# Optimization experiments

Measured on AMD Instinct MI355X. Metric: run time of the kernel, lower is better.

Reference implementation:

```python
import jax, jax.numpy as jnp
import numpy as np

TEMP = 0.5  # matches init_kwargs temperature


def setup_inputs() -> dict:
    key = jax.random.key(0)
    k1, k2 = jax.random.split(key)
    B, D = 4096, 256
    return {
        "z_i": jax.random.normal(k1, (B, D), dtype=jnp.float32),
        "z_j": jax.random.normal(k2, (B, D), dtype=jnp.float32),
    }


def reference(z_i, z_j):
    B = z_i.shape[0]
    N = 2 * B
    z = jnp.concatenate([z_i, z_j], axis=0)          # [N, D]
    sim = (z @ z.T) / TEMP                            # [N, N]

    # Faithful to source: BOTH positive halves come from diag(sim, +B)
    pos = jnp.concatenate([jnp.diagonal(sim, offset=B)] * 2)  # [N]

    # Arithmetic mask: exclude diagonal and the +/-B off-diagonals (static)
    idx = np.arange(N)
    mask = (idx[:, None] != idx[None, :]) & (np.abs(idx[:, None] - idx[None, :]) != B)
    neg = jnp.where(jnp.asarray(mask), sim, -jnp.inf)          # [N, N]

    # logits = [pos | negatives], label = 0 -> CE_i = lse(logits_i) - pos_i
    logits = jnp.concatenate([pos[:, None], neg], axis=1)      # [N, N+1]
    lse = jax.nn.logsumexp(logits, axis=1)                     # [N]
    loss = jnp.mean(lse - pos) / N                             # CE mean, then /N as in source
    return loss
```

## Files before the change

kernel.cpp:

```cpp
#include <hip/hip_runtime.h>
#include <hip/hip_bf16.h>

#define DD 256
#define NN 8192
#define B_ROWS 4096
#define G 64
#define NPAIRS 2080
#define M_FIX 160.0f
#define SCALE 1.6986436f
#define LN2 0.69314718055994531f

typedef __attribute__((ext_vector_type(8))) short bf16x8;
typedef __attribute__((ext_vector_type(4))) float f32x4;

__device__ __forceinline__ unsigned short f2bf(float f) {
    unsigned int x = __float_as_uint(f);
    x += 0x7fffu + ((x >> 16) & 1u);
    return (unsigned short)(x >> 16);
}
__device__ __forceinline__ float bf2f(unsigned short u) {
    return __uint_as_float((unsigned int)u << 16);
}
__device__ __forceinline__ float exp2_raw(float x) {
    float r; asm("v_exp_f32 %0, %1" : "=v"(r) : "v"(x)); return r;
}
__device__ __forceinline__ void gload16(const unsigned short* g, unsigned short* l) {
    __builtin_amdgcn_global_load_lds(
        (const __attribute__((address_space(1))) void*)g,
        (__attribute__((address_space(3))) void*)l, 16, 0, 0);
}

__global__ void cast_pos_kernel(const float* __restrict__ zi, const float* __restrict__ zj,
                                unsigned short* __restrict__ zb, float* __restrict__ pos) {
    const int w = threadIdx.x >> 6;
    const int l = threadIdx.x & 63;
    const int r = blockIdx.x * 4 + w;
    const float4 a = ((const float4*)(zi + (size_t)r * DD))[l];
    const float4 b = ((const float4*)(zj + (size_t)r * DD))[l];
    float d = a.x * b.x + a.y * b.y + a.z * b.z + a.w * b.w;
    #pragma unroll
    for (int off = 32; off > 0; off >>= 1) d += __shfl_down(d, off, 64);
    if (l == 0) pos[r] = 2.0f * d;
    ushort4 oa, ob;
    oa.x = f2bf(a.x * SCALE); oa.y = f2bf(a.y * SCALE);
    oa.z = f2bf(a.z * SCALE); oa.w = f2bf(a.w * SCALE);
    ob.x = f2bf(b.x * SCALE); ob.y = f2bf(b.y * SCALE);
    ob.z = f2bf(b.z * SCALE); ob.w = f2bf(b.w * SCALE);
    ((ushort4*)(zb + (size_t)r * DD))[l] = oa;
    ((ushort4*)(zb + (size_t)(r + B_ROWS) * DD))[l] = ob;
}

__global__ __launch_bounds__(128, 2) void simlse_kernel(const unsigned short* __restrict__ zb,
                                                        unsigned short* __restrict__ P) {
    __shared__ unsigned short tile[64 * DD];
    const int tid = threadIdx.x;
    const int w  = tid >> 6;
    const int l  = tid & 63;
    const int lg = l >> 4;
    const int lr = l & 15;

    int b = blockIdx.x, g1 = 0;
    while (b >= G - g1) { b -= G - g1; ++g1; }
    const int g2 = g1 + b;
    const int rbase = g1 * 128 + w * 64;
    const int cbase = g2 * 128;
    const bool diag = (g1 == g2);

    bf16x8 aF[4][8];
    #pragma unroll
    for (int rt = 0; rt < 4; ++rt) {
        const unsigned short* ap = zb + (size_t)(rbase + rt * 16 + lr) * DD + lg * 8;
        #pragma unroll
        for (int ks = 0; ks < 8; ++ks) aF[rt][ks] = *(const bf16x8*)(ap + ks * 32);
    }

    float rs[4][4];
    #pragma unroll
    for (int rt = 0; rt < 4; ++rt)
        #pragma unroll
        for (int j = 0; j < 4; ++j) rs[rt][j] = 0.f;
    float cs[8];
    #pragma unroll
    for (int k = 0; k < 8; ++k) cs[k] = 0.f;

    #pragma unroll
    for (int t = 0; t < 2; ++t) {
        const int c0 = cbase + t * 64;
        __syncthreads();
        #pragma unroll
        for (int j = 0; j < 16; ++j) {
            const int slot = w * 16 + j;
            const int s = slot >> 3, ks = slot & 7;
            gload16(zb + (size_t)(c0 + s * 16 + lr) * DD + ks * 32 + lg * 8,
                    tile + slot * 512);
        }
        __syncthreads();
        #pragma unroll
        for (int s = 0; s < 4; ++s) {
            f32x4 acc[4];
            #pragma unroll
            for (int rt = 0; rt < 4; ++rt) acc[rt] = (f32x4){0.f, 0.f, 0.f, 0.f};
            #pragma unroll
            for (int ks = 0; ks < 8; ++ks) {
                bf16x8 bF = *(const bf16x8*)(tile + (s * 8 + ks) * 512 + l * 8);
                #pragma unroll
                for (int rt = 0; rt < 4; ++rt)
                    acc[rt] = __builtin_amdgcn_mfma_f32_16x16x32_bf16(aF[rt][ks], bF, acc[rt], 0, 0, 0);
            }
            float csum = 0.f;
            #pragma unroll
            for (int rt = 0; rt < 4; ++rt) {
                const bool dtile = diag && (w * 4 + rt == t * 4 + s);
                #pragma unroll
                for (int j = 0; j < 4; ++j) {
                    float e = exp2_raw(acc[rt][j] - M_FIX);
                    if (dtile && (lr == lg * 4 + j)) e = 0.f;
                    rs[rt][j] += e;
                    csum += e;
                }
            }
            cs[t * 4 + s] = csum;
        }
    }

    #pragma unroll
    for (int rt = 0; rt < 4; ++rt)
        #pragma unroll
        for (int j = 0; j < 4; ++j) {
            float v = rs[rt][j];
            v += __shfl_xor(v, 1, 64);
            v += __shfl_xor(v, 2, 64);
            v += __shfl_xor(v, 4, 64);
            v += __shfl_xor(v, 8, 64);
            rs[rt][j] = v;
        }
    if (lr == 0) {
        #pragma unroll
        for (int rt = 0; rt < 4; ++rt)
            #pragma unroll
            for (int j = 0; j < 4; ++j) {
                const int row = rbase + rt * 16 + lg * 4 + j;
                P[(size_t)row * G + g2] = f2bf(rs[rt][j]);
            }
    }

    if (!diag) {
        #pragma unroll
        for (int k = 0; k < 8; ++k) {
            float v = cs[k];
            v += __shfl_xor(v, 16, 64);
            v += __shfl_xor(v, 32, 64);
            cs[k] = v;
        }
        __syncthreads();
        float* red = (float*)tile;
        if (lg == 0) {
            #pragma unroll
            for (int k = 0; k < 8; ++k) red[(w * 8 + k) * 16 + lr] = cs[k];
        }
        __syncthreads();
        const int k2 = tid >> 4, lr2 = tid & 15;
        float v = red[k2 * 16 + lr2] + red[(8 + k2) * 16 + lr2];
        P[(size_t)(cbase + tid) * G + g1] = f2bf(v);
    }
}

__global__ void rowmerge_kernel(const unsigned short* __restrict__ P,
                                const float* __restrict__ pos, float* __restrict__ partial) {
    const int r = blockIdx.x * 256 + threadIdx.x;
    float S = 0.f;
    const ushort4* p4 = (const ushort4*)(P + (size_t)r * G);
    #pragma unroll
    for (int k = 0; k < 16; ++k) {
        ushort4 u = p4[k];
        S += bf2f(u.x) + bf2f(u.y) + bf2f(u.z) + bf2f(u.w);
    }
    float val = M_FIX * LN2 + logf(S);
    if (r < B_ROWS) val -= 2.0f * pos[r];
    __shared__ float red[256];
    red[threadIdx.x] = val;
    __syncthreads();
    for (int st = 128; st > 0; st >>= 1) {
        if (threadIdx.x < st) red[threadIdx.x] += red[threadIdx.x + st];
        __syncthreads();
    }
    if (threadIdx.x == 0) partial[blockIdx.x] = red[0];
}

__global__ void final_kernel(const float* __restrict__ partial, float* __restrict__ out) {
    float v = (threadIdx.x < 32) ? partial[threadIdx.x] : 0.f;
    #pragma unroll
    for (int off = 32; off > 0; off >>= 1) v += __shfl_down(v, off, 64);
    if (threadIdx.x == 0) out[0] = v / (8192.f * 8192.f);
}

extern "C" void kernel_launch(void* const* d_in, const int* in_sizes, int n_in,
                              void* d_out, int out_size, void* d_ws, size_t ws_size,
                              hipStream_t stream) {
    const float* zi = (const float*)d_in[0];
    const float* zj = (const float*)d_in[1];
    float* out = (float*)d_out;
    char* ws = (char*)d_ws;

    unsigned short* zb = (unsigned short*)ws;
    unsigned short* P  = (unsigned short*)(ws + (size_t)NN * DD * 2);
    float* pos     = (float*)(ws + (size_t)NN * DD * 2 + (size_t)NN * G * 2);
    float* partial = pos + B_ROWS;

    hipLaunchKernelGGL(cast_pos_kernel, dim3(B_ROWS / 4), dim3(256), 0, stream, zi, zj, zb, pos);
    hipLaunchKernelGGL(simlse_kernel,   dim3(NPAIRS), dim3(128), 0, stream, zb, P);
    hipLaunchKernelGGL(rowmerge_kernel, dim3(NN / 256), dim3(256), 0, stream, P, pos, partial);
    hipLaunchKernelGGL(final_kernel,    dim3(1), dim3(64), 0, stream, partial, out);
}
```

Before: 66.43 us.

## Enlarge symmetric sim tiles to 256x256 with four waves and transpose partial-sum layout

The symmetric block-pair tiling now uses 256-row groups (32 groups, 528 pairs) with 256-thread blocks, so each loaded column tile is reused by four waves. Fewer and larger blocks cut redundant global loads and the partial-sum count per row. The partial-sum buffer is stored group-major so both the row and column writes and the merge reads are coalesced. In exchange, 528 blocks give coarser load balance across CUs, the outer t loop is no longer unrolled, and the kernel carries more column-sum registers.

Result: faster. 56.79 us (-14.5%).

```diff
diff --git a/kernel.cpp b/kernel.cpp
--- a/kernel.cpp
+++ b/kernel.cpp
@@ -4,8 +4,9 @@
 #define DD 256
 #define NN 8192
 #define B_ROWS 4096
-#define G 64
-#define NPAIRS 2080
+#define G 32
+#define GSZ 256
+#define NPAIRS 528
 #define M_FIX 160.0f
 #define SCALE 1.6986436f
 #define LN2 0.69314718055994531f
@@ -50,9 +51,9 @@
     ((ushort4*)(zb + (size_t)(r + B_ROWS) * DD))[l] = ob;
 }
 
-__global__ __launch_bounds__(128, 2) void simlse_kernel(const unsigned short* __restrict__ zb,
-                                                        unsigned short* __restrict__ P) {
-    __shared__ unsigned short tile[64 * DD];
+__global__ __launch_bounds__(256, 2) void simlse_kernel(const unsigned short* __restrict__ zb,
+                                                        unsigned short* __restrict__ PT) {
+    __shared__ unsigned short tile[32 * 512];
     const int tid = threadIdx.x;
     const int w  = tid >> 6;
     const int l  = tid & 63;
@@ -62,9 +63,9 @@
     int b = blockIdx.x, g1 = 0;
     while (b >= G - g1) { b -= G - g1; ++g1; }
     const int g2 = g1 + b;
-    const int rbase = g1 * 128 + w * 64;
-    const int cbase = g2 * 128;
     const bool diag = (g1 == g2);
+    const int rbase = g1 * GSZ + w * 64;
+    const int cbase = g2 * GSZ;
 
     bf16x8 aF[4][8];
     #pragma unroll
@@ -79,24 +80,21 @@
     for (int rt = 0; rt < 4; ++rt)
         #pragma unroll
         for (int j = 0; j < 4; ++j) rs[rt][j] = 0.f;
-    float cs[8];
-    #pragma unroll
-    for (int k = 0; k < 8; ++k) cs[k] = 0.f;
-
-    #pragma unroll
-    for (int t = 0; t < 2; ++t) {
+    float cs[16];
+    #pragma unroll
+    for (int k = 0; k < 16; ++k) cs[k] = 0.f;
+
+    for (int t = 0; t < 4; ++t) {
         const int c0 = cbase + t * 64;
         __syncthreads();
         #pragma unroll
-        for (int j = 0; j < 16; ++j) {
-            const int slot = w * 16 + j;
-            const int s = slot >> 3, ks = slot & 7;
-            gload16(zb + (size_t)(c0 + s * 16 + lr) * DD + ks * 32 + lg * 8,
-                    tile + slot * 512);
-        }
+        for (int j = 0; j < 8; ++j)
+            gload16(zb + (size_t)(c0 + w * 16 + lr) * DD + j * 32 + lg * 8,
+                    tile + (w * 8 + j) * 512);
         __syncthreads();
         #pragma unroll
         for (int s = 0; s < 4; ++s) {
+            const int ct = t * 4 + s;
             f32x4 acc[4];
             #pragma unroll
             for (int rt = 0; rt < 4; ++rt) acc[rt] = (f32x4){0.f, 0.f, 0.f, 0.f};
@@ -107,19 +105,17 @@
                 for (int rt = 0; rt < 4; ++rt)
                     acc[rt] = __builtin_amdgcn_mfma_f32_16x16x32_bf16(aF[rt][ks], bF, acc[rt], 0, 0, 0);
             }
-            float csum = 0.f;
             #pragma unroll
             for (int rt = 0; rt < 4; ++rt) {
-                const bool dtile = diag && (w * 4 + rt == t * 4 + s);
+                const bool dt = diag && (w * 4 + rt == ct);
                 #pragma unroll
                 for (int j = 0; j < 4; ++j) {
                     float e = exp2_raw(acc[rt][j] - M_FIX);
-                    if (dtile && (lr == lg * 4 + j)) e = 0.f;
+                    if (dt && (lr == lg * 4 + j)) e = 0.f;
                     rs[rt][j] += e;
-                    csum += e;
+                    cs[ct] += e;
                 }
             }
-            cs[t * 4 + s] = csum;
         }
     }
 
@@ -138,15 +134,13 @@
         #pragma unroll
         for (int rt = 0; rt < 4; ++rt)
             #pragma unroll
-            for (int j = 0; j < 4; ++j) {
-                const int row = rbase + rt * 16 + lg * 4 + j;
-                P[(size_t)row * G + g2] = f2bf(rs[rt][j]);
-            }
+            for (int j = 0; j < 4; ++j)
+                PT[(size_t)g2 * NN + rbase + rt * 16 + lg * 4 + j] = f2bf(rs[rt][j]);
     }
 
     if (!diag) {
         #pragma unroll
-        for (int k = 0; k < 8; ++k) {
+        for (int k = 0; k < 16; ++k) {
             float v = cs[k];
             v += __shfl_xor(v, 16, 64);
             v += __shfl_xor(v, 32, 64);
@@ -156,25 +150,20 @@
         float* red = (float*)tile;
         if (lg == 0) {
             #pragma unroll
-            for (int k = 0; k < 8; ++k) red[(w * 8 + k) * 16 + lr] = cs[k];
-        }
-        __syncthreads();
-        const int k2 = tid >> 4, lr2 = tid & 15;
-        float v = red[k2 * 16 + lr2] + red[(8 + k2) * 16 + lr2];
-        P[(size_t)(cbase + tid) * G + g1] = f2bf(v);
-    }
-}
-
-__global__ void rowmerge_kernel(const unsigned short* __restrict__ P,
+            for (int k = 0; k < 16; ++k) red[w * 256 + k * 16 + lr] = cs[k];
+        }
+        __syncthreads();
+        const float v = red[tid] + red[256 + tid] + red[512 + tid] + red[768 + tid];
+        PT[(size_t)g1 * NN + cbase + tid] = f2bf(v);
+    }
+}
+
+__global__ void rowmerge_kernel(const unsigned short* __restrict__ PT,
                                 const float* __restrict__ pos, float* __restrict__ partial) {
     const int r = blockIdx.x * 256 + threadIdx.x;
     float S = 0.f;
-    const ushort4* p4 = (const ushort4*)(P + (size_t)r * G);
-    #pragma unroll
-    for (int k = 0; k < 16; ++k) {
-        ushort4 u = p4[k];
-        S += bf2f(u.x) + bf2f(u.y) + bf2f(u.z) + bf2f(u.w);
-    }
+    #pragma unroll
+    for (int c = 0; c < G; ++c) S += bf2f(PT[(size_t)c * NN + r]);
     float val = M_FIX * LN2 + logf(S);
     if (r < B_ROWS) val -= 2.0f * pos[r];
     __shared__ float red[256];
@@ -203,12 +192,12 @@
     char* ws = (char*)d_ws;
 
     unsigned short* zb = (unsigned short*)ws;
-    unsigned short* P  = (unsigned short*)(ws + (size_t)NN * DD * 2);
-    float* pos     = (float*)(ws + (size_t)NN * DD * 2 + (size_t)NN * G * 2);
+    unsigned short* PT = (unsigned short*)(ws + (size_t)NN * DD * 2);
+    float* pos     = (float*)(ws + (size_t)NN * DD * 2 + (size_t)G * NN * 2);
     float* partial = pos + B_ROWS;
 
     hipLaunchKernelGGL(cast_pos_kernel, dim3(B_ROWS / 4), dim3(256), 0, stream, zi, zj, zb, pos);
-    hipLaunchKernelGGL(simlse_kernel,   dim3(NPAIRS), dim3(128), 0, stream, zb, P);
-    hipLaunchKernelGGL(rowmerge_kernel, dim3(NN / 256), dim3(256), 0, stream, P, pos, partial);
+    hipLaunchKernelGGL(simlse_kernel,   dim3(NPAIRS), dim3(256), 0, stream, zb, PT);
+    hipLaunchKernelGGL(rowmerge_kernel, dim3(NN / 256), dim3(256), 0, stream, PT, pos, partial);
     hipLaunchKernelGGL(final_kernel,    dim3(1), dim3(64), 0, stream, partial, out);
 }
```
